# Optimization experiments

Measured on AMD Instinct MI355X. Metric: run time of the kernel, lower is better.

## Reference

```python
import jax, jax.numpy as jnp
import numpy as np

B, S, E = 2, 2048, 1024
H, BLK = 16, 32
HD = E // H


def setup_inputs() -> dict:
    key = jax.random.key(0)
    ks = jax.random.split(key, 9)
    s = 1.0 / np.sqrt(E)
    return {
        "x": jax.random.normal(ks[0], (B, S, E), dtype=jnp.float32),
        "Wq": jax.random.normal(ks[1], (E, E), dtype=jnp.float32) * s,
        "bq": jnp.zeros((E,), dtype=jnp.float32),
        "Wk": jax.random.normal(ks[2], (E, E), dtype=jnp.float32) * s,
        "bk": jnp.zeros((E,), dtype=jnp.float32),
        "Wv": jax.random.normal(ks[3], (E, E), dtype=jnp.float32) * s,
        "bv": jnp.zeros((E,), dtype=jnp.float32),
        "Wo": jax.random.normal(ks[4], (E, E), dtype=jnp.float32) * s,
        "bo": jnp.zeros((E,), dtype=jnp.float32),
    }


def reference(x, Wq, bq, Wk, bk, Wv, bv, Wo, bo):
    b, s, e = x.shape
    # projections (torch Linear: x @ W.T + b), split heads -> [b, h, s, hd]
    def proj(W, bias):
        return (x @ W.T + bias).reshape(b, s, H, HD).transpose(0, 2, 1, 3)

    q = proj(Wq, bq)
    k = proj(Wk, bk)
    v = proj(Wv, bv)

    scale = 1.0 / np.sqrt(HD)
    scores = jnp.einsum("bhqd,bhkd->bhqk", q, k) * scale  # [b,h,s,s]

    # block-causal mask: query block i attends to all key blocks j <= i
    idx = jnp.arange(s)
    allowed = (idx[None, :] // BLK) <= (idx[:, None] // BLK)  # [s, s]
    scores = jnp.where(allowed[None, None], scores, jnp.float32(-1e9))

    probs = jax.nn.softmax(scores, axis=-1)
    attn = jnp.einsum("bhqk,bhkd->bhqd", probs, v)  # [b,h,s,hd]
    out = attn.transpose(0, 2, 1, 3).reshape(b, s, e)
    return out @ Wo.T + bo
```

## Files before the change

### kernel.cpp

```cpp
#include <hip/hip_runtime.h>
#include <hip/hip_bf16.h>
#include <stdint.h>

#define BATCH 2
#define S_LEN 2048
#define EMB   1024
#define NHEAD 16
#define HDIM  64

typedef __attribute__((ext_vector_type(8)))  __bf16 bf16x8;
typedef __attribute__((ext_vector_type(4)))  __bf16 bf16x4;
typedef __attribute__((ext_vector_type(4)))  float  f32x4;
typedef __attribute__((ext_vector_type(16))) float  f32x16;

#define ZERO16 ((f32x16){0.f,0.f,0.f,0.f,0.f,0.f,0.f,0.f,0.f,0.f,0.f,0.f,0.f,0.f,0.f,0.f})
#define SM_SCALE_LOG2 0.18033688011112042f

static __device__ __forceinline__ void gload_lds16(const void* g, void* l) {
    __builtin_amdgcn_global_load_lds(
        (__attribute__((address_space(1))) void*)g,
        (__attribute__((address_space(3))) void*)l,
        16, 0, 0);
}

__global__ void f2b_all(const float* __restrict__ x,
                        const float* __restrict__ Wq, const float* __restrict__ Wk,
                        const float* __restrict__ Wv, const float* __restrict__ Wo,
                        __bf16* __restrict__ xb,
                        __bf16* __restrict__ wqb, __bf16* __restrict__ wkb,
                        __bf16* __restrict__ wvb, __bf16* __restrict__ wob) {
    int i = blockIdx.x * blockDim.x + threadIdx.x;
    const float* s;
    __bf16* d;
    int off;
    if (i < (1 << 20)) {
        s = x; d = xb; off = i;
    } else {
        int r   = i - (1 << 20);
        int seg = r >> 18;
        off = r & ((1 << 18) - 1);
        s = seg == 0 ? Wq : seg == 1 ? Wk : seg == 2 ? Wv : Wo;
        d = seg == 0 ? wqb : seg == 1 ? wkb : seg == 2 ? wvb : wob;
    }
    float4 v = reinterpret_cast<const float4*>(s)[off];
    bf16x4 o = { (__bf16)v.x, (__bf16)v.y, (__bf16)v.z, (__bf16)v.w };
    reinterpret_cast<bf16x4*>(d)[off] = o;
}

__global__ __launch_bounds__(256)
void gemm_o64(const __bf16* __restrict__ A, const __bf16* __restrict__ W,
              const float* __restrict__ bias, float* __restrict__ out,
              int M, int N, int K) {
    __shared__ __align__(16) __bf16 As[2][128 * 32];
    __shared__ __align__(16) __bf16 Bs[2][64 * 32];

    const int t    = threadIdx.x;
    const int w    = t >> 6;
    const int lane = t & 63;
    const int m0   = blockIdx.y * 128;
    const int n0   = blockIdx.x * 64;
    const int wr   = w * 32;
    const int fr   = lane & 15;
    const int kg   = (lane >> 4) * 8;

    f32x4 acc[2][4];
#pragma unroll
    for (int i = 0; i < 2; ++i)
#pragma unroll
        for (int n = 0; n < 4; ++n) acc[i][n] = (f32x4){0.f, 0.f, 0.f, 0.f};

    auto stage = [&](int kt, int buf) {
#pragma unroll
        for (int i = 0; i < 2; ++i) {
            int chunk = i * 256 + t;
            int row   = chunk >> 2;
            int col   = (chunk & 3) * 8;
            gload_lds16(A + (size_t)(m0 + row) * K + kt + col,
                        (char*)&As[buf][0] + i * 4096 + w * 1024);
        }
        {
            int row = t >> 2;
            int col = (t & 3) * 8;
            gload_lds16(W + (size_t)(n0 + row) * K + kt + col,
                        (char*)&Bs[buf][0] + w * 1024);
        }
    };

    stage(0, 0);
    __syncthreads();

    const int NK = K / 32;
    for (int k6 = 0; k6 < NK; ++k6) {
        const int cur = k6 & 1;
        if (k6 + 1 < NK) stage((k6 + 1) * 32, cur ^ 1);

        bf16x8 af[2], bfv[4];
#pragma unroll
        for (int m = 0; m < 2; ++m)
            af[m] = *(const bf16x8*)&As[cur][(wr + m * 16 + fr) * 32 + kg];
#pragma unroll
        for (int n = 0; n < 4; ++n)
            bfv[n] = *(const bf16x8*)&Bs[cur][(n * 16 + fr) * 32 + kg];
#pragma unroll
        for (int m = 0; m < 2; ++m)
#pragma unroll
            for (int n = 0; n < 4; ++n)
                acc[m][n] = __builtin_amdgcn_mfma_f32_16x16x32_bf16(
                    af[m], bfv[n], acc[m][n], 0, 0, 0);
        __syncthreads();
    }

    const int rbase = (lane >> 4) * 4;
#pragma unroll
    for (int m = 0; m < 2; ++m) {
#pragma unroll
        for (int n = 0; n < 4; ++n) {
            int col  = n0 + n * 16 + fr;
            float bv = bias[col];
#pragma unroll
            for (int jj = 0; jj < 4; ++jj) {
                int row = m0 + wr + m * 16 + rbase + jj;
                out[(size_t)row * N + col] = acc[m][n][jj] + bv;
            }
        }
    }
}

__global__ __launch_bounds__(256)
void gemm_qkv(const __bf16* __restrict__ xb,
              const __bf16* __restrict__ Wqb, const __bf16* __restrict__ Wkb,
              const __bf16* __restrict__ Wvb,
              const float* __restrict__ bqp, const float* __restrict__ bkp,
              const float* __restrict__ bvp,
              __bf16* __restrict__ Qo, __bf16* __restrict__ Ko,
              __bf16* __restrict__ VTo, int K) {
    __shared__ __align__(16) __bf16 As[2][128 * 32];
    __shared__ __align__(16) __bf16 Bs[2][128 * 32];

    const int which = blockIdx.x >> 3;
    const int xx    = blockIdx.x & 7;

    const __bf16* Ap;
    const __bf16* Wp;
    int m0, n0;
    if (which == 2) {
        Ap = Wvb; Wp = xb;
        m0 = xx * 128;
        n0 = blockIdx.y * 128;
    } else {
        Ap = xb; Wp = (which == 0) ? Wqb : Wkb;
        m0 = blockIdx.y * 128;
        n0 = xx * 128;
    }
    const float* bias = which == 0 ? bqp : which == 1 ? bkp : bvp;

    const int t    = threadIdx.x;
    const int w    = t >> 6;
    const int lane = t & 63;
    const int wr   = (w >> 1) * 64;
    const int wc   = (w & 1) * 64;
    const int fr   = lane & 15;
    const int kg   = (lane >> 4) * 8;

    f32x4 acc[4][4];
#pragma unroll
    for (int i = 0; i < 4; ++i)
#pragma unroll
        for (int j = 0; j < 4; ++j) acc[i][j] = (f32x4){0.f, 0.f, 0.f, 0.f};

    auto stage = [&](int kt, int buf) {
#pragma unroll
        for (int i = 0; i < 2; ++i) {
            int chunk = i * 256 + t;
            int row   = chunk >> 2;
            int col   = (chunk & 3) * 8;
            gload_lds16(Ap + (size_t)(m0 + row) * K + kt + col,
                        (char*)&As[buf][0] + i * 4096 + w * 1024);
            gload_lds16(Wp + (size_t)(n0 + row) * K + kt + col,
                        (char*)&Bs[buf][0] + i * 4096 + w * 1024);
        }
    };

    stage(0, 0);
    __syncthreads();

    const int NK = K / 32;
    for (int k6 = 0; k6 < NK; ++k6) {
        const int cur = k6 & 1;
        if (k6 + 1 < NK) stage((k6 + 1) * 32, cur ^ 1);

        bf16x8 af[4], bfv[4];
#pragma unroll
        for (int m = 0; m < 4; ++m)
            af[m] = *(const bf16x8*)&As[cur][(wr + m * 16 + fr) * 32 + kg];
#pragma unroll
        for (int n = 0; n < 4; ++n)
            bfv[n] = *(const bf16x8*)&Bs[cur][(wc + n * 16 + fr) * 32 + kg];
#pragma unroll
        for (int m = 0; m < 4; ++m)
#pragma unroll
            for (int n = 0; n < 4; ++n)
                acc[m][n] = __builtin_amdgcn_mfma_f32_16x16x32_bf16(
                    af[m], bfv[n], acc[m][n], 0, 0, 0);
        __syncthreads();
    }

    const int rbase = (lane >> 4) * 4;
    if (which == 2) {
#pragma unroll
        for (int m = 0; m < 4; ++m) {
#pragma unroll
            for (int n = 0; n < 4; ++n) {
                int col = n0 + wc + n * 16 + fr;
                int b   = col >> 11, s = col & (S_LEN - 1);
#pragma unroll
                for (int jj = 0; jj < 4; ++jj) {
                    int row = m0 + wr + m * 16 + rbase + jj;
                    int hh  = row >> 6, d = row & (HDIM - 1);
                    float v = acc[m][n][jj] + bias[row];
                    VTo[(((size_t)(b * NHEAD + hh)) * HDIM + d) * S_LEN + s] = (__bf16)v;
                }
            }
        }
    } else {
        __bf16* outp = (which == 0) ? Qo : Ko;
#pragma unroll
        for (int m = 0; m < 4; ++m) {
#pragma unroll
            for (int n = 0; n < 4; ++n) {
                int col  = n0 + wc + n * 16 + fr;
                float bv = bias[col];
#pragma unroll
                for (int jj = 0; jj < 4; ++jj) {
                    int row = m0 + wr + m * 16 + rbase + jj;
                    float v = acc[m][n][jj] + bv;
                    int b = row >> 11, s = row & (S_LEN - 1);
                    int hh = col >> 6, d = col & (HDIM - 1);
                    outp[(((size_t)(b * NHEAD + hh)) * S_LEN + s) * HDIM + d] = (__bf16)v;
                }
            }
        }
    }
}

__global__ __launch_bounds__(512, 4)
void attn7_kernel(const __bf16* __restrict__ Q, const __bf16* __restrict__ Kv,
                  const __bf16* __restrict__ VT, __bf16* __restrict__ out) {
    __shared__ __align__(16) char smem[51200];
    __bf16* Kt0 = (__bf16*)smem;
    __bf16* Vt  = (__bf16*)(smem + 32768);
    float*  bc  = (float*)(smem + 49152);

    const int t    = threadIdx.x;
    const int w8   = t >> 6;
    const int lane = t & 63;
    const int h    = lane >> 5;
    const int q32  = lane & 31;
    const int j    = w8 & 1;
    const int h4   = w8 >> 1;
    const int bh   = blockIdx.x;
    const int qt   = 31 - blockIdx.y;
    const int qb   = 2 * qt + j;
    const int C    = (2 * qt + 5) >> 2;

    const __bf16* Qp  = Q  + (size_t)bh * S_LEN * HDIM;
    const __bf16* Kp  = Kv + (size_t)bh * S_LEN * HDIM;
    const __bf16* VTp = VT + (size_t)bh * HDIM * S_LEN;

    const int qrow = qb * 32 + q32;

    bf16x8 qreg[4];
#pragma unroll
    for (int ks = 0; ks < 4; ++ks)
        qreg[ks] = *(const bf16x8*)&Qp[(size_t)qrow * HDIM + 16 * ks + 8 * h];

    f32x16 oacc0 = ZERO16, oacc1 = ZERO16;
    float mrun = -1e30f, lrun = 0.f;

    {
#pragma unroll
        for (int i = 0; i < 2; ++i) {
            int c16 = i * 512 + t;
            int key = c16 >> 3;
            int d0  = ((c16 & 7) ^ (key & 7)) * 8;
            gload_lds16(Kp + (size_t)key * HDIM + d0, (char*)Kt0 + c16 * 16);
        }
        __syncthreads();
    }

    for (int c = 0; c < C; ++c) {
        const int cur = c & 1;
        {
            const int kb = c * 128;
#pragma unroll
            for (int i = 0; i < 2; ++i) {
                int c16 = i * 512 + t;
                int d   = c16 >> 4;
                int o   = c16 & 15;
                gload_lds16(VTp + (size_t)d * S_LEN + kb + ((o ^ (d & 7)) * 8),
                            (char*)Vt + c16 * 16);
            }
        }
        if (c + 1 < C) {
            const int kb = (c + 1) * 128;
#pragma unroll
            for (int i = 0; i < 2; ++i) {
                int c16 = i * 512 + t;
                int key = c16 >> 3;
                int d0  = ((c16 & 7) ^ (key & 7)) * 8;
                gload_lds16(Kp + (size_t)(kb + key) * HDIM + d0,
                            (char*)Kt0 + (cur ^ 1) * 16384 + c16 * 16);
            }
        }

        const bool work = (4 * c + h4 <= qb);
        unsigned L[4], H[4];

        if (work) {
            const __bf16* Ktc = Kt0 + cur * 8192;
            const int klocal = 32 * h4;

            f32x16 sac = ZERO16;
            __builtin_amdgcn_s_setprio(1);
#pragma unroll
            for (int ks = 0; ks < 4; ++ks) {
                bf16x8 kf = *(const bf16x8*)&Ktc[(klocal + q32) * 64 +
                                ((16 * ks + 8 * h) ^ ((q32 & 7) << 3))];
                sac = __builtin_amdgcn_mfma_f32_32x32x16_bf16(kf, qreg[ks], sac, 0, 0, 0);
            }
            __builtin_amdgcn_s_setprio(0);

            float rmax = sac[0];
#pragma unroll
            for (int r = 1; r < 16; ++r) rmax = fmaxf(rmax, sac[r]);
            float pmax = rmax * SM_SCALE_LOG2;
            pmax = fmaxf(pmax, __shfl_xor(pmax, 32));

            if (__any(pmax > mrun + 8.f)) {
                float mnew = fmaxf(mrun, pmax);
                float fac  = exp2f(mrun - mnew);
                mrun = mnew;
                lrun *= fac;
                bc[w8 * 32 + q32] = fac;
                asm volatile("s_waitcnt lgkmcnt(0)" ::: "memory");
                __builtin_amdgcn_sched_barrier(0);
#pragma unroll
                for (int q2 = 0; q2 < 4; ++q2) {
                    f32x4 fv = *(const f32x4*)&bc[w8 * 32 + 8 * q2 + 4 * h];
#pragma unroll
                    for (int jj = 0; jj < 4; ++jj) {
                        oacc0[4 * q2 + jj] *= fv[jj];
                        oacc1[4 * q2 + jj] *= fv[jj];
                    }
                }
            }

            float ps = 0.f;
#pragma unroll
            for (int r = 0; r < 16; ++r) {
                float pv = exp2f(__builtin_fmaf(sac[r], SM_SCALE_LOG2, -mrun));
                ps += pv;
                sac[r] = pv;
            }
            ps += __shfl_xor(ps, 32);
            lrun += ps;

#pragma unroll
            for (int g = 0; g < 4; ++g) {
                asm("v_cvt_pk_bf16_f32 %0, %1, %2"
                    : "=v"(L[g]) : "v"(sac[4 * g]), "v"(sac[4 * g + 1]));
                asm("v_cvt_pk_bf16_f32 %0, %1, %2"
                    : "=v"(H[g]) : "v"(sac[4 * g + 2]), "v"(sac[4 * g + 3]));
            }
        }

        __syncthreads();

        if (work) {
            const int klocal = 32 * h4;
            __builtin_amdgcn_s_setprio(1);
#pragma unroll
            for (int s2 = 0; s2 < 2; ++s2) {
                unsigned a0 = L[2 * s2], b0 = L[2 * s2 + 1];
                unsigned a1 = H[2 * s2], b1 = H[2 * s2 + 1];
                asm("v_permlane32_swap_b32 %0, %1" : "+v"(a0), "+v"(b0));
                asm("v_permlane32_swap_b32 %0, %1" : "+v"(a1), "+v"(b1));
                unsigned wvw[4] = { a0, a1, b0, b1 };
                bf16x8 pa = *(bf16x8*)wvw;

                const int klb = klocal + 16 * s2 + 8 * h;
#pragma unroll
                for (int n = 0; n < 2; ++n) {
                    int d = 32 * n + q32;
                    bf16x8 vf = *(const bf16x8*)&Vt[d * 128 +
                                    (klb ^ ((d & 7) << 3))];
                    if (n == 0)
                        oacc0 = __builtin_amdgcn_mfma_f32_32x32x16_bf16(pa, vf, oacc0, 0, 0, 0);
                    else
                        oacc1 = __builtin_amdgcn_mfma_f32_32x32x16_bf16(pa, vf, oacc1, 0, 0, 0);
                }
            }
            __builtin_amdgcn_s_setprio(0);
        }

        __syncthreads();
    }

    float* Oex = (float*)smem;
    float* MLm = (float*)(smem + 49152);
    float* MLl = (float*)(smem + 50176);

    if (h == 0) { MLm[w8 * 32 + q32] = mrun; MLl[w8 * 32 + q32] = lrun; }
    if (h4 != 0) {
        float* ob = Oex + (j * 3 + h4 - 1) * 2048;
#pragma unroll
        for (int q2 = 0; q2 < 4; ++q2)
#pragma unroll
            for (int jj = 0; jj < 4; ++jj) {
                int r  = 4 * q2 + jj;
                int rl = 8 * q2 + 4 * h + jj;
                ob[rl * 64 + q32]      = oacc0[r];
                ob[rl * 64 + 32 + q32] = oacc1[r];
            }
    }
    __syncthreads();

    if (h4 == 0) {
        const int b = bh >> 4, hh = bh & (NHEAD - 1);
        __bf16* op = out + (size_t)b * S_LEN * EMB + hh * HDIM;
        const float* ob1 = Oex + (j * 3 + 0) * 2048;
        const float* ob2 = Oex + (j * 3 + 1) * 2048;
        const float* ob3 = Oex + (j * 3 + 2) * 2048;
#pragma unroll
        for (int q2 = 0; q2 < 4; ++q2) {
            f32x4 mv[4], lv[4];
#pragma unroll
            for (int p = 0; p < 4; ++p) {
                int wp = (p << 1) | j;
                mv[p] = *(const f32x4*)&MLm[wp * 32 + 8 * q2 + 4 * h];
                lv[p] = *(const f32x4*)&MLl[wp * 32 + 8 * q2 + 4 * h];
            }
#pragma unroll
            for (int jj = 0; jj < 4; ++jj) {
                float mst = fmaxf(fmaxf(mv[0][jj], mv[1][jj]),
                                  fmaxf(mv[2][jj], mv[3][jj]));
                float s0 = exp2f(mv[0][jj] - mst);
                float s1 = exp2f(mv[1][jj] - mst);
                float s2 = exp2f(mv[2][jj] - mst);
                float s3 = exp2f(mv[3][jj] - mst);
                float inv = 1.f / (lv[0][jj] * s0 + lv[1][jj] * s1 +
                                   lv[2][jj] * s2 + lv[3][jj] * s3);
                int r  = 4 * q2 + jj;
                int rl = 8 * q2 + 4 * h + jj;
                int row = qb * 32 + rl;
                float v0 = (oacc0[r] * s0 + ob1[rl * 64 + q32] * s1 +
                            ob2[rl * 64 + q32] * s2 + ob3[rl * 64 + q32] * s3) * inv;
                float v1 = (oacc1[r] * s0 + ob1[rl * 64 + 32 + q32] * s1 +
                            ob2[rl * 64 + 32 + q32] * s2 + ob3[rl * 64 + 32 + q32] * s3) * inv;
                op[(size_t)row * EMB + q32]      = (__bf16)v0;
                op[(size_t)row * EMB + 32 + q32] = (__bf16)v1;
            }
        }
    }
}

extern "C" void kernel_launch(void* const* d_in, const int* in_sizes, int n_in,
                              void* d_out, int out_size, void* d_ws, size_t ws_size,
                              hipStream_t stream) {
    const float* x  = (const float*)d_in[0];
    const float* Wq = (const float*)d_in[1];
    const float* bq = (const float*)d_in[2];
    const float* Wk = (const float*)d_in[3];
    const float* bk = (const float*)d_in[4];
    const float* Wv = (const float*)d_in[5];
    const float* bv = (const float*)d_in[6];
    const float* Wo = (const float*)d_in[7];
    const float* bo = (const float*)d_in[8];
    float* out = (float*)d_out;

    char* ws = (char*)d_ws;
    __bf16* xb  = (__bf16*)(ws + 0);
    __bf16* wqb = (__bf16*)(ws + 8388608);
    __bf16* wkb = (__bf16*)(ws + 10485760);
    __bf16* wvb = (__bf16*)(ws + 12582912);
    __bf16* wob = (__bf16*)(ws + 14680064);
    __bf16* Qb  = (__bf16*)(ws + 16777216);
    __bf16* Kb  = (__bf16*)(ws + 25165824);
    __bf16* VTb = (__bf16*)(ws + 33554432);
    __bf16* Ab  = (__bf16*)(ws + 41943040);

    const int M = BATCH * S_LEN;
    const int N = EMB;
    const int K = EMB;

    f2b_all<<<8192, 256, 0, stream>>>(x, Wq, Wk, Wv, Wo, xb, wqb, wkb, wvb, wob);

    gemm_qkv<<<dim3(24, 32), 256, 0, stream>>>(
        xb, wqb, wkb, wvb, bq, bk, bv, Qb, Kb, VTb, K);

    attn7_kernel<<<dim3(BATCH * NHEAD, 32), 512, 0, stream>>>(Qb, Kb, VTb, Ab);

    gemm_o64<<<dim3(16, M / 128), 256, 0, stream>>>(Ab, wob, bo, out, M, N, K);
}
```

Before: 123.2 us.

## Load K/V fragments directly from global into registers, drop LDS staging and barriers

The attention kernel no longer stages K and V^T tiles cooperatively through LDS with per-chunk __syncthreads. Each wave now walks its own strided set of key blocks, loading K fragments straight from global memory into registers with double buffering, and loading V fragments the same way. This removes the block-wide barriers and lets waves proceed independently, which also balances causal work per wave. The cost is more global/L2 traffic, since each wave rereads K/V instead of sharing it through LDS, plus uncoalesced strided V^T loads.

```diff
diff --git a/kernel.cpp b/kernel.cpp
--- a/kernel.cpp
+++ b/kernel.cpp
@@ -244,12 +244,10 @@
 }
 
 __global__ __launch_bounds__(512, 4)
-void attn7_kernel(const __bf16* __restrict__ Q, const __bf16* __restrict__ Kv,
+void attn8_kernel(const __bf16* __restrict__ Q, const __bf16* __restrict__ Kv,
                   const __bf16* __restrict__ VT, __bf16* __restrict__ out) {
     __shared__ __align__(16) char smem[51200];
-    __bf16* Kt0 = (__bf16*)smem;
-    __bf16* Vt  = (__bf16*)(smem + 32768);
-    float*  bc  = (float*)(smem + 49152);
+    float* bc = (float*)(smem + 49152);
 
     const int t    = threadIdx.x;
     const int w8   = t >> 6;
@@ -261,7 +259,6 @@
     const int bh   = blockIdx.x;
     const int qt   = 31 - blockIdx.y;
     const int qb   = 2 * qt + j;
-    const int C    = (2 * qt + 5) >> 2;
 
     const __bf16* Qp  = Q  + (size_t)bh * S_LEN * HDIM;
     const __bf16* Kp  = Kv + (size_t)bh * S_LEN * HDIM;
@@ -277,139 +274,109 @@
     f32x16 oacc0 = ZERO16, oacc1 = ZERO16;
     float mrun = -1e30f, lrun = 0.f;
 
+    auto loadK = [&](int i, bf16x8* dst) {
+#pragma unroll
+        for (int ks = 0; ks < 4; ++ks)
+            dst[ks] = *(const bf16x8*)&Kp[(size_t)(i * 32 + q32) * 64 + 16 * ks + 8 * h];
+    };
+
+    auto step = [&](int i, const bf16x8* kf) {
+        f32x16 sac = ZERO16;
+        __builtin_amdgcn_s_setprio(1);
+#pragma unroll
+        for (int ks = 0; ks < 4; ++ks)
+            sac = __builtin_amdgcn_mfma_f32_32x32x16_bf16(kf[ks], qreg[ks], sac, 0, 0, 0);
+        __builtin_amdgcn_s_setprio(0);
+
+        bf16x8 vf0[2], vf1[2];
+#pragma unroll
+        for (int s2 = 0; s2 < 2; ++s2) {
+            vf0[s2] = *(const bf16x8*)&VTp[(size_t)q32 * S_LEN + 32 * i + 16 * s2 + 8 * h];
+            vf1[s2] = *(const bf16x8*)&VTp[(size_t)(32 + q32) * S_LEN + 32 * i + 16 * s2 + 8 * h];
+        }
+
+        float rmax = sac[0];
+#pragma unroll
+        for (int r = 1; r < 16; ++r) rmax = fmaxf(rmax, sac[r]);
+        float pmax = rmax * SM_SCALE_LOG2;
+        pmax = fmaxf(pmax, __shfl_xor(pmax, 32));
+
+        if (__any(pmax > mrun + 8.f)) {
+            float mnew = fmaxf(mrun, pmax);
+            float fac  = exp2f(mrun - mnew);
+            mrun = mnew;
+            lrun *= fac;
+            bc[w8 * 32 + q32] = fac;
+            asm volatile("s_waitcnt lgkmcnt(0)" ::: "memory");
+            __builtin_amdgcn_sched_barrier(0);
+#pragma unroll
+            for (int q2 = 0; q2 < 4; ++q2) {
+                f32x4 fv = *(const f32x4*)&bc[w8 * 32 + 8 * q2 + 4 * h];
+#pragma unroll
+                for (int jj = 0; jj < 4; ++jj) {
+                    oacc0[4 * q2 + jj] *= fv[jj];
+                    oacc1[4 * q2 + jj] *= fv[jj];
+                }
+            }
+        }
+
+        float ps = 0.f;
+#pragma unroll
+        for (int r = 0; r < 16; ++r) {
+            float pv = exp2f(__builtin_fmaf(sac[r], SM_SCALE_LOG2, -mrun));
+            ps += pv;
+            sac[r] = pv;
+        }
+        ps += __shfl_xor(ps, 32);
+        lrun += ps;
+
+        unsigned L[4], H[4];
+#pragma unroll
+        for (int g = 0; g < 4; ++g) {
+            asm("v_cvt_pk_bf16_f32 %0, %1, %2"
+                : "=v"(L[g]) : "v"(sac[4 * g]), "v"(sac[4 * g + 1]));
+            asm("v_cvt_pk_bf16_f32 %0, %1, %2"
+                : "=v"(H[g]) : "v"(sac[4 * g + 2]), "v"(sac[4 * g + 3]));
+        }
+
+        __builtin_amdgcn_s_setprio(1);
+#pragma unroll
+        for (int s2 = 0; s2 < 2; ++s2) {
+            unsigned a0 = L[2 * s2], b0 = L[2 * s2 + 1];
+            unsigned a1 = H[2 * s2], b1 = H[2 * s2 + 1];
+            asm("v_permlane32_swap_b32 %0, %1" : "+v"(a0), "+v"(b0));
+            asm("v_permlane32_swap_b32 %0, %1" : "+v"(a1), "+v"(b1));
+            unsigned wvw[4] = { a0, a1, b0, b1 };
+            bf16x8 pa = *(bf16x8*)wvw;
+            oacc0 = __builtin_amdgcn_mfma_f32_32x32x16_bf16(pa, vf0[s2], oacc0, 0, 0, 0);
+            oacc1 = __builtin_amdgcn_mfma_f32_32x32x16_bf16(pa, vf1[s2], oacc1, 0, 0, 0);
+        }
+        __builtin_amdgcn_s_setprio(0);
+    };
+
     {
-#pragma unroll
-        for (int i = 0; i < 2; ++i) {
-            int c16 = i * 512 + t;
-            int key = c16 >> 3;
-            int d0  = ((c16 & 7) ^ (key & 7)) * 8;
-            gload_lds16(Kp + (size_t)key * HDIM + d0, (char*)Kt0 + c16 * 16);
-        }
-        __syncthreads();
-    }
-
-    for (int c = 0; c < C; ++c) {
-        const int cur = c & 1;
-        {
-            const int kb = c * 128;
-#pragma unroll
-            for (int i = 0; i < 2; ++i) {
-                int c16 = i * 512 + t;
-                int d   = c16 >> 4;
-                int o   = c16 & 15;
-                gload_lds16(VTp + (size_t)d * S_LEN + kb + ((o ^ (d & 7)) * 8),
-                            (char*)Vt + c16 * 16);
-            }
-        }
-        if (c + 1 < C) {
-            const int kb = (c + 1) * 128;
-#pragma unroll
-            for (int i = 0; i < 2; ++i) {
-                int c16 = i * 512 + t;
-                int key = c16 >> 3;
-                int d0  = ((c16 & 7) ^ (key & 7)) * 8;
-                gload_lds16(Kp + (size_t)(kb + key) * HDIM + d0,
-                            (char*)Kt0 + (cur ^ 1) * 16384 + c16 * 16);
-            }
-        }
-
-        const bool work = (4 * c + h4 <= qb);
-        unsigned L[4], H[4];
-
-        if (work) {
-            const __bf16* Ktc = Kt0 + cur * 8192;
-            const int klocal = 32 * h4;
-
-            f32x16 sac = ZERO16;
-            __builtin_amdgcn_s_setprio(1);
-#pragma unroll
-            for (int ks = 0; ks < 4; ++ks) {
-                bf16x8 kf = *(const bf16x8*)&Ktc[(klocal + q32) * 64 +
-                                ((16 * ks + 8 * h) ^ ((q32 & 7) << 3))];
-                sac = __builtin_amdgcn_mfma_f32_32x32x16_bf16(kf, qreg[ks], sac, 0, 0, 0);
-            }
-            __builtin_amdgcn_s_setprio(0);
-
-            float rmax = sac[0];
-#pragma unroll
-            for (int r = 1; r < 16; ++r) rmax = fmaxf(rmax, sac[r]);
-            float pmax = rmax * SM_SCALE_LOG2;
-            pmax = fmaxf(pmax, __shfl_xor(pmax, 32));
-
-            if (__any(pmax > mrun + 8.f)) {
-                float mnew = fmaxf(mrun, pmax);
-                float fac  = exp2f(mrun - mnew);
-                mrun = mnew;
-                lrun *= fac;
-                bc[w8 * 32 + q32] = fac;
-                asm volatile("s_waitcnt lgkmcnt(0)" ::: "memory");
-                __builtin_amdgcn_sched_barrier(0);
-#pragma unroll
-                for (int q2 = 0; q2 < 4; ++q2) {
-                    f32x4 fv = *(const f32x4*)&bc[w8 * 32 + 8 * q2 + 4 * h];
-#pragma unroll
-                    for (int jj = 0; jj < 4; ++jj) {
-                        oacc0[4 * q2 + jj] *= fv[jj];
-                        oacc1[4 * q2 + jj] *= fv[jj];
-                    }
-                }
-            }
-
-            float ps = 0.f;
-#pragma unroll
-            for (int r = 0; r < 16; ++r) {
-                float pv = exp2f(__builtin_fmaf(sac[r], SM_SCALE_LOG2, -mrun));
-                ps += pv;
-                sac[r] = pv;
-            }
-            ps += __shfl_xor(ps, 32);
-            lrun += ps;
-
-#pragma unroll
-            for (int g = 0; g < 4; ++g) {
-                asm("v_cvt_pk_bf16_f32 %0, %1, %2"
-                    : "=v"(L[g]) : "v"(sac[4 * g]), "v"(sac[4 * g + 1]));
-                asm("v_cvt_pk_bf16_f32 %0, %1, %2"
-                    : "=v"(H[g]) : "v"(sac[4 * g + 2]), "v"(sac[4 * g + 3]));
-            }
-        }
-
-        __syncthreads();
-
-        if (work) {
-            const int klocal = 32 * h4;
-            __builtin_amdgcn_s_setprio(1);
-#pragma unroll
-            for (int s2 = 0; s2 < 2; ++s2) {
-                unsigned a0 = L[2 * s2], b0 = L[2 * s2 + 1];
-                unsigned a1 = H[2 * s2], b1 = H[2 * s2 + 1];
-                asm("v_permlane32_swap_b32 %0, %1" : "+v"(a0), "+v"(b0));
-                asm("v_permlane32_swap_b32 %0, %1" : "+v"(a1), "+v"(b1));
-                unsigned wvw[4] = { a0, a1, b0, b1 };
-                bf16x8 pa = *(bf16x8*)wvw;
-
-                const int klb = klocal + 16 * s2 + 8 * h;
-#pragma unroll
-                for (int n = 0; n < 2; ++n) {
-                    int d = 32 * n + q32;
-                    bf16x8 vf = *(const bf16x8*)&Vt[d * 128 +
-                                    (klb ^ ((d & 7) << 3))];
-                    if (n == 0)
-                        oacc0 = __builtin_amdgcn_mfma_f32_32x32x16_bf16(pa, vf, oacc0, 0, 0, 0);
-                    else
-                        oacc1 = __builtin_amdgcn_mfma_f32_32x32x16_bf16(pa, vf, oacc1, 0, 0, 0);
-                }
-            }
-            __builtin_amdgcn_s_setprio(0);
-        }
-
-        __syncthreads();
+        bf16x8 ka[4], kn[4];
+        int i = h4;
+        if (i <= qb) {
+            loadK(i, ka);
+            for (;;) {
+                if (i + 4 <= qb) loadK(i + 4, kn);
+                step(i, ka);
+                i += 4;
+                if (i > qb) break;
+                if (i + 4 <= qb) loadK(i + 4, ka);
+                step(i, kn);
+                i += 4;
+                if (i > qb) break;
+            }
+        }
     }
 
     float* Oex = (float*)smem;
     float* MLm = (float*)(smem + 49152);
     float* MLl = (float*)(smem + 50176);
 
+    __syncthreads();
     if (h == 0) { MLm[w8 * 32 + q32] = mrun; MLl[w8 * 32 + q32] = lrun; }
     if (h4 != 0) {
         float* ob = Oex + (j * 3 + h4 - 1) * 2048;
@@ -498,7 +465,7 @@
     gemm_qkv<<<dim3(24, 32), 256, 0, stream>>>(
         xb, wqb, wkb, wvb, bq, bk, bv, Qb, Kb, VTb, K);
 
-    attn7_kernel<<<dim3(BATCH * NHEAD, 32), 512, 0, stream>>>(Qb, Kb, VTb, Ab);
+    attn8_kernel<<<dim3(BATCH * NHEAD, 32), 512, 0, stream>>>(Qb, Kb, VTb, Ab);
 
     gemm_o64<<<dim3(16, M / 128), 256, 0, stream>>>(Ab, wob, bo, out, M, N, K);
 }
```

Result: slower. 204.0 us (+65.5%).

## Widen attention tile to 128 query rows with two key sub-blocks per wave

Applied to the files above, without the earlier changes.

The attention kernel now covers four 32-row query blocks per workgroup instead of two. Each wave handles two consecutive 32-key sub-blocks per 128-key chunk rather than one, and the grid is halved to 16 query tiles per head, ordered to interleave heavy and light tiles. Each loaded K/V chunk is reused by twice as many query rows and the final cross-wave merge combines two partial results instead of four. In exchange there are half as many blocks to fill the GPU, each wave carries a longer serial chain with more branch divergence at the causal diagonal, and the online-softmax state is updated twice per chunk.

```diff
diff --git a/kernel.cpp b/kernel.cpp
--- a/kernel.cpp
+++ b/kernel.cpp
@@ -244,8 +244,8 @@
 }
 
 __global__ __launch_bounds__(512, 4)
-void attn7_kernel(const __bf16* __restrict__ Q, const __bf16* __restrict__ Kv,
-                  const __bf16* __restrict__ VT, __bf16* __restrict__ out) {
+void attn10_kernel(const __bf16* __restrict__ Q, const __bf16* __restrict__ Kv,
+                   const __bf16* __restrict__ VT, __bf16* __restrict__ out) {
     __shared__ __align__(16) char smem[51200];
     __bf16* Kt0 = (__bf16*)smem;
     __bf16* Vt  = (__bf16*)(smem + 32768);
@@ -256,12 +256,13 @@
     const int lane = t & 63;
     const int h    = lane >> 5;
     const int q32  = lane & 31;
-    const int j    = w8 & 1;
-    const int h4   = w8 >> 1;
+    const int j    = w8 & 3;
+    const int h2   = w8 >> 2;
     const int bh   = blockIdx.x;
-    const int qt   = 31 - blockIdx.y;
-    const int qb   = 2 * qt + j;
-    const int C    = (2 * qt + 5) >> 2;
+    const int yy   = blockIdx.y;
+    const int qt   = (yy < 8) ? (15 - yy) : (yy - 8);
+    const int qb   = 4 * qt + j;
+    const int C    = qt + 1;
 
     const __bf16* Qp  = Q  + (size_t)bh * S_LEN * HDIM;
     const __bf16* Kp  = Kv + (size_t)bh * S_LEN * HDIM;
@@ -313,18 +314,19 @@
             }
         }
 
-        const bool work = (4 * c + h4 <= qb);
+        const int  g0 = 4 * c + 2 * h2;
+        const bool w0 = (g0 <= qb);
+        const bool w1 = (g0 + 1 <= qb);
+        const int  kl0 = 64 * h2;
+        const __bf16* Ktc = Kt0 + cur * 8192;
+
         unsigned L[4], H[4];
-
-        if (work) {
-            const __bf16* Ktc = Kt0 + cur * 8192;
-            const int klocal = 32 * h4;
-
+        if (w0) {
             f32x16 sac = ZERO16;
             __builtin_amdgcn_s_setprio(1);
 #pragma unroll
             for (int ks = 0; ks < 4; ++ks) {
-                bf16x8 kf = *(const bf16x8*)&Ktc[(klocal + q32) * 64 +
+                bf16x8 kf = *(const bf16x8*)&Ktc[(kl0 + q32) * 64 +
                                 ((16 * ks + 8 * h) ^ ((q32 & 7) << 3))];
                 sac = __builtin_amdgcn_mfma_f32_32x32x16_bf16(kf, qreg[ks], sac, 0, 0, 0);
             }
@@ -376,8 +378,7 @@
 
         __syncthreads();
 
-        if (work) {
-            const int klocal = 32 * h4;
+        if (w0) {
             __builtin_amdgcn_s_setprio(1);
 #pragma unroll
             for (int s2 = 0; s2 < 2; ++s2) {
@@ -388,7 +389,7 @@
                 unsigned wvw[4] = { a0, a1, b0, b1 };
                 bf16x8 pa = *(bf16x8*)wvw;
 
-                const int klb = klocal + 16 * s2 + 8 * h;
+                const int klb = kl0 + 16 * s2 + 8 * h;
 #pragma unroll
                 for (int n = 0; n < 2; ++n) {
                     int d = 32 * n + q32;
@@ -403,6 +404,87 @@
             __builtin_amdgcn_s_setprio(0);
         }
 
+        if (w1) {
+            const int kl1 = kl0 + 32;
+            f32x16 sac = ZERO16;
+            __builtin_amdgcn_s_setprio(1);
+#pragma unroll
+            for (int ks = 0; ks < 4; ++ks) {
+                bf16x8 kf = *(const bf16x8*)&Ktc[(kl1 + q32) * 64 +
+                                ((16 * ks + 8 * h) ^ ((q32 & 7) << 3))];
+                sac = __builtin_amdgcn_mfma_f32_32x32x16_bf16(kf, qreg[ks], sac, 0, 0, 0);
+            }
+            __builtin_amdgcn_s_setprio(0);
+
+            float rmax = sac[0];
+#pragma unroll
+            for (int r = 1; r < 16; ++r) rmax = fmaxf(rmax, sac[r]);
+            float pmax = rmax * SM_SCALE_LOG2;
+            pmax = fmaxf(pmax, __shfl_xor(pmax, 32));
+
+            if (__any(pmax > mrun + 8.f)) {
+                float mnew = fmaxf(mrun, pmax);
+                float fac  = exp2f(mrun - mnew);
+                mrun = mnew;
+                lrun *= fac;
+                bc[w8 * 32 + q32] = fac;
+                asm volatile("s_waitcnt lgkmcnt(0)" ::: "memory");
+                __builtin_amdgcn_sched_barrier(0);
+#pragma unroll
+                for (int q2 = 0; q2 < 4; ++q2) {
+                    f32x4 fv = *(const f32x4*)&bc[w8 * 32 + 8 * q2 + 4 * h];
+#pragma unroll
+                    for (int jj = 0; jj < 4; ++jj) {
+                        oacc0[4 * q2 + jj] *= fv[jj];
+                        oacc1[4 * q2 + jj] *= fv[jj];
+                    }
+                }
+            }
+
+            float ps = 0.f;
+#pragma unroll
+            for (int r = 0; r < 16; ++r) {
+                float pv = exp2f(__builtin_fmaf(sac[r], SM_SCALE_LOG2, -mrun));
+                ps += pv;
+                sac[r] = pv;
+            }
+            ps += __shfl_xor(ps, 32);
+            lrun += ps;
+
+            unsigned L1[4], H1[4];
+#pragma unroll
+            for (int g = 0; g < 4; ++g) {
+                asm("v_cvt_pk_bf16_f32 %0, %1, %2"
+                    : "=v"(L1[g]) : "v"(sac[4 * g]), "v"(sac[4 * g + 1]));
+                asm("v_cvt_pk_bf16_f32 %0, %1, %2"
+                    : "=v"(H1[g]) : "v"(sac[4 * g + 2]), "v"(sac[4 * g + 3]));
+            }
+
+            __builtin_amdgcn_s_setprio(1);
+#pragma unroll
+            for (int s2 = 0; s2 < 2; ++s2) {
+                unsigned a0 = L1[2 * s2], b0 = L1[2 * s2 + 1];
+                unsigned a1 = H1[2 * s2], b1 = H1[2 * s2 + 1];
+                asm("v_permlane32_swap_b32 %0, %1" : "+v"(a0), "+v"(b0));
+                asm("v_permlane32_swap_b32 %0, %1" : "+v"(a1), "+v"(b1));
+                unsigned wvw[4] = { a0, a1, b0, b1 };
+                bf16x8 pa = *(bf16x8*)wvw;
+
+                const int klb = kl1 + 16 * s2 + 8 * h;
+#pragma unroll
+                for (int n = 0; n < 2; ++n) {
+                    int d = 32 * n + q32;
+                    bf16x8 vf = *(const bf16x8*)&Vt[d * 128 +
+                                    (klb ^ ((d & 7) << 3))];
+                    if (n == 0)
+                        oacc0 = __builtin_amdgcn_mfma_f32_32x32x16_bf16(pa, vf, oacc0, 0, 0, 0);
+                    else
+                        oacc1 = __builtin_amdgcn_mfma_f32_32x32x16_bf16(pa, vf, oacc1, 0, 0, 0);
+                }
+            }
+            __builtin_amdgcn_s_setprio(0);
+        }
+
         __syncthreads();
     }
 
@@ -411,8 +493,8 @@
     float* MLl = (float*)(smem + 50176);
 
     if (h == 0) { MLm[w8 * 32 + q32] = mrun; MLl[w8 * 32 + q32] = lrun; }
-    if (h4 != 0) {
-        float* ob = Oex + (j * 3 + h4 - 1) * 2048;
+    if (h2 == 1) {
+        float* ob = Oex + j * 2048;
 #pragma unroll
         for (int q2 = 0; q2 < 4; ++q2)
 #pragma unroll
@@ -425,38 +507,27 @@
     }
     __syncthreads();
 
-    if (h4 == 0) {
+    if (h2 == 0) {
         const int b = bh >> 4, hh = bh & (NHEAD - 1);
         __bf16* op = out + (size_t)b * S_LEN * EMB + hh * HDIM;
-        const float* ob1 = Oex + (j * 3 + 0) * 2048;
-        const float* ob2 = Oex + (j * 3 + 1) * 2048;
-        const float* ob3 = Oex + (j * 3 + 2) * 2048;
+        const float* ob = Oex + j * 2048;
 #pragma unroll
         for (int q2 = 0; q2 < 4; ++q2) {
-            f32x4 mv[4], lv[4];
-#pragma unroll
-            for (int p = 0; p < 4; ++p) {
-                int wp = (p << 1) | j;
-                mv[p] = *(const f32x4*)&MLm[wp * 32 + 8 * q2 + 4 * h];
-                lv[p] = *(const f32x4*)&MLl[wp * 32 + 8 * q2 + 4 * h];
-            }
+            f32x4 ma4 = *(const f32x4*)&MLm[j * 32 + 8 * q2 + 4 * h];
+            f32x4 mb4 = *(const f32x4*)&MLm[(j + 4) * 32 + 8 * q2 + 4 * h];
+            f32x4 la4 = *(const f32x4*)&MLl[j * 32 + 8 * q2 + 4 * h];
+            f32x4 lb4 = *(const f32x4*)&MLl[(j + 4) * 32 + 8 * q2 + 4 * h];
 #pragma unroll
             for (int jj = 0; jj < 4; ++jj) {
-                float mst = fmaxf(fmaxf(mv[0][jj], mv[1][jj]),
-                                  fmaxf(mv[2][jj], mv[3][jj]));
-                float s0 = exp2f(mv[0][jj] - mst);
-                float s1 = exp2f(mv[1][jj] - mst);
-                float s2 = exp2f(mv[2][jj] - mst);
-                float s3 = exp2f(mv[3][jj] - mst);
-                float inv = 1.f / (lv[0][jj] * s0 + lv[1][jj] * s1 +
-                                   lv[2][jj] * s2 + lv[3][jj] * s3);
+                float ma = ma4[jj], mb = mb4[jj];
+                float mst = fmaxf(ma, mb);
+                float sa  = exp2f(ma - mst), sb = exp2f(mb - mst);
+                float inv = 1.f / (la4[jj] * sa + lb4[jj] * sb);
                 int r  = 4 * q2 + jj;
                 int rl = 8 * q2 + 4 * h + jj;
                 int row = qb * 32 + rl;
-                float v0 = (oacc0[r] * s0 + ob1[rl * 64 + q32] * s1 +
-                            ob2[rl * 64 + q32] * s2 + ob3[rl * 64 + q32] * s3) * inv;
-                float v1 = (oacc1[r] * s0 + ob1[rl * 64 + 32 + q32] * s1 +
-                            ob2[rl * 64 + 32 + q32] * s2 + ob3[rl * 64 + 32 + q32] * s3) * inv;
+                float v0 = (oacc0[r] * sa + ob[rl * 64 + q32] * sb) * inv;
+                float v1 = (oacc1[r] * sa + ob[rl * 64 + 32 + q32] * sb) * inv;
                 op[(size_t)row * EMB + q32]      = (__bf16)v0;
                 op[(size_t)row * EMB + 32 + q32] = (__bf16)v1;
             }
@@ -498,7 +569,7 @@
     gemm_qkv<<<dim3(24, 32), 256, 0, stream>>>(
         xb, wqb, wkb, wvb, bq, bk, bv, Qb, Kb, VTb, K);
 
-    attn7_kernel<<<dim3(BATCH * NHEAD, 32), 512, 0, stream>>>(Qb, Kb, VTb, Ab);
+    attn10_kernel<<<dim3(BATCH * NHEAD, 16), 512, 0, stream>>>(Qb, Kb, VTb, Ab);
 
     gemm_o64<<<dim3(16, M / 128), 256, 0, stream>>>(Ab, wob, bo, out, M, N, K);
 }
```

New measurement: 120.0 us. 2.6% less time.
